# Kernel tuning notes

Hardware: AMD Instinct MI355X
Metric: run time of the kernel (lower is better)

## Reference

```python
import jax, jax.numpy as jnp
import numpy as np

N = 100000          # nodes
E = 3200000         # edges (avg degree 32)
F_IN = 128          # num_features
HID = 128           # hidden_channels
C = 8               # num_classes
G = 64              # graphs in batch
EPS = 1e-5


def setup_inputs() -> dict:
    key = jax.random.key(0)
    ks = jax.random.split(key, 10)
    x = jax.random.normal(ks[0], (N, F_IN), dtype=jnp.float32)
    edge_index = jax.random.randint(ks[1], (2, E), 0, N, dtype=jnp.int64)
    batch = jnp.sort(jax.random.randint(ks[2], (N,), 0, G, dtype=jnp.int64))
    # parameters
    glorot1 = float(np.sqrt(6.0 / (F_IN + HID)))
    W1 = jax.random.uniform(ks[3], (F_IN, HID), minval=-glorot1, maxval=glorot1, dtype=jnp.float32)
    conv1_bias = jnp.zeros((HID,), jnp.float32)
    bn_weight = jnp.ones((F_IN,), jnp.float32)
    bn_bias = jnp.zeros((F_IN,), jnp.float32)
    ln_weight = jnp.ones((HID,), jnp.float32)
    ln_bias = jnp.zeros((HID,), jnp.float32)
    glorot2 = float(np.sqrt(6.0 / (HID + C)))
    lin_W = jax.random.uniform(ks[4], (C, HID), minval=-glorot2, maxval=glorot2, dtype=jnp.float32)
    lin_b = jnp.zeros((C,), jnp.float32)
    return {"x": x, "edge_index": edge_index, "batch": batch,
            "bn_weight": bn_weight, "bn_bias": bn_bias,
            "W1": W1, "conv1_bias": conv1_bias,
            "ln_weight": ln_weight, "ln_bias": ln_bias,
            "lin_W": lin_W, "lin_b": lin_b}


def reference(x, edge_index, batch, bn_weight, bn_bias, W1, conv1_bias,
              ln_weight, ln_bias, lin_W, lin_b):
    n = x.shape[0]
    # BatchNorm1d over nodes (training-mode batch statistics, biased var)
    mu = x.mean(axis=0)
    var = x.var(axis=0)
    x = (x - mu) * jax.lax.rsqrt(var + EPS) * bn_weight + bn_bias
    # GCNConv: linear transform, add self-loops, symmetric normalization, scatter-add
    h = x @ W1                                   # [N, HID]
    loops = jnp.arange(n, dtype=edge_index.dtype)
    row = jnp.concatenate([edge_index[0], loops])  # source nodes
    col = jnp.concatenate([edge_index[1], loops])  # target nodes
    deg = jax.ops.segment_sum(jnp.ones_like(col, dtype=h.dtype), col, num_segments=N)
    dinv = jax.lax.rsqrt(deg)                    # deg >= 1 due to self-loops
    norm = dinv[row] * dinv[col]                 # [E+N]
    msg = h[row] * norm[:, None]                 # gather + scale
    h = jax.ops.segment_sum(msg, col, num_segments=N) + conv1_bias
    h = jax.nn.relu(h)
    # PyG LayerNorm, mode='graph', batch=None: normalize over the whole tensor
    h = h - h.mean()
    h = h * jax.lax.rsqrt(h.var() + EPS)
    h = h * ln_weight + ln_bias
    # global mean pool per graph
    counts = jax.ops.segment_sum(jnp.ones((n,), h.dtype), batch, num_segments=G)
    sums = jax.ops.segment_sum(h, batch, num_segments=G)
    g = sums / jnp.maximum(counts, 1.0)[:, None]  # [G, HID]
    return g @ lin_W.T + lin_b                    # [G, C]
```

## Files before the change

kernel.cpp:

```cpp
#include <hip/hip_runtime.h>

#define NN 100000
#define NE 3200000
#define F 128
#define NG 64
#define NC 8
#define EPSF 1e-5f

#define AGG_BLOCKS 25000
#define LDSTRIDE 136
#define BN_BLOCKS 1024

#define NBK 256
#define BNODES 391
#define BCAP 14336
#define CHUNK 4096
#define P1_BLOCKS ((NE + CHUNK - 1) / CHUNK)

typedef __attribute__((ext_vector_type(8))) short bf16x8;
typedef __attribute__((ext_vector_type(4))) float f32x4;
typedef _Float16 f16x2 __attribute__((ext_vector_type(2)));

union U32H2 { unsigned int u; f16x2 h; };
__device__ __forceinline__ f16x2 asH2(unsigned int u) { U32H2 c; c.u = u; return c.h; }
__device__ __forceinline__ unsigned int asU32(f16x2 h) { U32H2 c; c.h = h; return c.u; }

__device__ __forceinline__ unsigned short f2bf(float f) {
    unsigned int u = __float_as_uint(f);
    u = u + 0x7FFFu + ((u >> 16) & 1u);
    return (unsigned short)(u >> 16);
}
__device__ __forceinline__ unsigned short f2h_bits(float f) {
    union { _Float16 h; unsigned short u; } c;
    c.h = (_Float16)f;
    return c.u;
}

__global__ void bn_partial_k(const float* __restrict__ x, float* __restrict__ part,
                             int n, int rpb) {
    int tid = threadIdx.x, col = tid & 127, half = tid >> 7;
    int r0 = blockIdx.x * rpb, r1 = min(n, r0 + rpb);
    float s = 0.f, ss = 0.f;
    for (int r = r0 + half; r < r1; r += 2) {
        float v = x[(size_t)r * F + col];
        s += v; ss += v * v;
    }
    __shared__ float sh[512];
    sh[tid] = s; sh[256 + tid] = ss;
    __syncthreads();
    if (half == 0) {
        part[blockIdx.x * 256 + col]       = sh[col] + sh[col + 128];
        part[blockIdx.x * 256 + 128 + col] = sh[256 + col] + sh[256 + col + 128];
    }
}

__global__ void bn_finalize_k(const float* __restrict__ part,
                              const float* __restrict__ bnw, const float* __restrict__ bnb,
                              float* __restrict__ scale, float* __restrict__ shift, int n) {
    int col = blockIdx.x, tid = threadIdx.x;
    float s = 0.f, ss = 0.f;
    #pragma unroll
    for (int i = 0; i < 4; ++i) {
        int b = tid + i * 256;
        s  += part[b * 256 + col];
        ss += part[b * 256 + 128 + col];
    }
    __shared__ float shs[256], shss[256];
    shs[tid] = s; shss[tid] = ss;
    __syncthreads();
    for (int o = 128; o > 0; o >>= 1) {
        if (tid < o) { shs[tid] += shs[tid + o]; shss[tid] += shss[tid + o]; }
        __syncthreads();
    }
    if (tid == 0) {
        float mu  = shs[0] / (float)n;
        float var = shss[0] / (float)n - mu * mu;
        float rstd = rsqrtf(var + EPSF);
        float sc = bnw[col] * rstd;
        scale[col] = sc;
        shift[col] = bnb[col] - mu * sc;
    }
}

__global__ void prep_wpT_k(const float* __restrict__ W1, const float* __restrict__ scale,
                           unsigned short* __restrict__ WpT) {
    int idx = blockIdx.x * 256 + threadIdx.x;
    if (idx < F * F) {
        int k = idx >> 7, j = idx & 127;
        WpT[j * F + k] = f2bf(scale[k] * W1[idx]);
    }
}
__global__ void prep_s_k(const float* __restrict__ W1, const float* __restrict__ shift,
                         float* __restrict__ S) {
    int j = blockIdx.x, k = threadIdx.x;
    __shared__ float sh[128];
    sh[k] = shift[k] * W1[k * F + j];
    __syncthreads();
    for (int o = 64; o > 0; o >>= 1) {
        if (k < o) sh[k] += sh[k + o];
        __syncthreads();
    }
    if (k == 0) S[j] = sh[0];
}

__global__ __launch_bounds__(256) void bucket_k(const int* __restrict__ ei,
                                                int* __restrict__ bcur,
                                                unsigned int* __restrict__ bbuf) {
    __shared__ int cntl[NBK];
    __shared__ int basel[NBK];
    __shared__ int gbase[NBK];
    __shared__ unsigned int ent[CHUNK];
    __shared__ unsigned char bid[CHUNK];
    int tid = threadIdx.x;
    int e0 = blockIdx.x * CHUNK;
    int ecnt = min(NE - e0, CHUNK);
    cntl[tid] = 0;
    __syncthreads();
    int myr[16], myc[16], myl[16];
    #pragma unroll
    for (int k = 0; k < 16; ++k) {
        int i = tid + k * 256;
        if (i < ecnt) {
            int r = ei[e0 + i];
            int c = ei[NE + e0 + i];
            myr[k] = r; myc[k] = c;
            myl[k] = atomicAdd(&cntl[(unsigned)c / BNODES], 1);
        } else { myr[k] = -1; myc[k] = 0; myl[k] = 0; }
    }
    __syncthreads();
    int myv = cntl[tid];
    basel[tid] = myv;
    __syncthreads();
    for (int o = 1; o < 256; o <<= 1) {
        int t = (tid >= o) ? basel[tid - o] : 0;
        __syncthreads();
        basel[tid] += t;
        __syncthreads();
    }
    basel[tid] -= myv;
    gbase[tid] = atomicAdd(&bcur[tid], myv);
    __syncthreads();
    #pragma unroll
    for (int k = 0; k < 16; ++k) {
        if (myr[k] >= 0) {
            int b = (unsigned)myc[k] / BNODES;
            int s = basel[b] + myl[k];
            ent[s] = ((unsigned)myr[k] << 9) | (unsigned)(myc[k] - b * BNODES);
            bid[s] = (unsigned char)b;
        }
    }
    __syncthreads();
    for (int s = tid; s < ecnt; s += 256) {
        unsigned int v = ent[s];
        int b = bid[s];
        int idx = s - basel[b] + gbase[b];
        if (idx < BCAP) bbuf[(size_t)b * BCAP + idx] = v;
    }
}

__global__ void bbase_k(const int* __restrict__ bcur, int* __restrict__ bbase,
                        int* __restrict__ offs) {
    int tid = threadIdx.x;
    __shared__ int s[256];
    int v = bcur[tid];
    s[tid] = v;
    __syncthreads();
    for (int o = 1; o < 256; o <<= 1) {
        int t = (tid >= o) ? s[tid - o] : 0;
        __syncthreads();
        s[tid] += t;
        __syncthreads();
    }
    bbase[tid] = s[tid] - v;
    if (tid == 255) offs[NN] = s[255];
}

__global__ void hist2_k(const unsigned int* __restrict__ bbuf, const int* __restrict__ bcur,
                        const int* __restrict__ bbase,
                        int* __restrict__ offs, float* __restrict__ dinv) {
    int b = blockIdx.x, tid = threadIdx.x;
    __shared__ int h0[512], hA[512], hB[512];
    h0[tid] = 0; h0[tid + 256] = 0;
    __syncthreads();
    int m = min(bcur[b], BCAP);
    for (int i = tid; i < m; i += 256)
        atomicAdd(&h0[bbuf[(size_t)b * BCAP + i] & 511u], 1);
    __syncthreads();
    hA[tid] = h0[tid]; hA[tid + 256] = h0[tid + 256];
    __syncthreads();
    int* src = hA; int* dst = hB;
    for (int o = 1; o < 512; o <<= 1) {
        int i0 = tid, i1 = tid + 256;
        dst[i0] = src[i0] + ((i0 >= o) ? src[i0 - o] : 0);
        dst[i1] = src[i1] + ((i1 >= o) ? src[i1 - o] : 0);
        __syncthreads();
        int* tmp = src; src = dst; dst = tmp;
    }
    int nbase = b * BNODES;
    int base = bbase[b];
    int lim = min(BNODES, NN - nbase);
    for (int i = tid; i < lim; i += 256) {
        int d = h0[i];
        offs[nbase + i] = base + src[i] - d;
        dinv[nbase + i] = rsqrtf((float)d + 1.0f);
    }
}

__global__ void scatter2_k(const unsigned int* __restrict__ bbuf, const int* __restrict__ bcur,
                           const int* __restrict__ offs, int* __restrict__ srow) {
    int b = blockIdx.x, tid = threadIdx.x;
    __shared__ int cur[BNODES];
    for (int i = tid; i < BNODES; i += 256) cur[i] = 0;
    __syncthreads();
    int nbase = b * BNODES;
    int m = min(bcur[b], BCAP);
    for (int i = tid; i < m; i += 256) {
        unsigned int v = bbuf[(size_t)b * BCAP + i];
        int dstl = (int)(v & 511u);
        int pos = offs[nbase + dstl] + atomicAdd(&cur[dstl], 1);
        srow[pos] = (int)(v >> 9);
    }
}

__global__ __launch_bounds__(256) void gemm_k(const float* __restrict__ x,
                                              const unsigned short* __restrict__ WpT,
                                              const float* __restrict__ S,
                                              const float* __restrict__ dinv,
                                              unsigned short* __restrict__ hf, int n) {
    __shared__ unsigned short wt[128 * LDSTRIDE];
    __shared__ unsigned short xt[64 * LDSTRIDE];
    int tid = threadIdx.x;
    int row0 = blockIdx.x * 64;
    for (int i = tid; i < 2048; i += 256) {
        int r = i >> 4, c = (i & 15) * 8;
        uint4 v = *(const uint4*)&WpT[r * F + c];
        *(uint4*)&wt[r * LDSTRIDE + c] = v;
    }
    for (int i = tid; i < 2048; i += 256) {
        int r = i >> 5, c = (i & 31) * 4;
        float4 v = make_float4(0.f, 0.f, 0.f, 0.f);
        if (row0 + r < n) v = *(const float4*)&x[(size_t)(row0 + r) * F + c];
        unsigned int p0 = (unsigned int)f2bf(v.x) | ((unsigned int)f2bf(v.y) << 16);
        unsigned int p1 = (unsigned int)f2bf(v.z) | ((unsigned int)f2bf(v.w) << 16);
        *(uint2*)&xt[r * LDSTRIDE + c] = make_uint2(p0, p1);
    }
    __syncthreads();
    int wv = tid >> 6, lane = tid & 63;
    int lm = lane & 15, lk = lane >> 4;
    bf16x8 afrag[4];
    #pragma unroll
    for (int kk = 0; kk < 4; ++kk)
        afrag[kk] = *(bf16x8*)&xt[(wv * 16 + lm) * LDSTRIDE + kk * 32 + lk * 8];
    float dv[4];
    #pragma unroll
    for (int j = 0; j < 4; ++j) {
        int r = row0 + wv * 16 + lk * 4 + j;
        dv[j] = (r < n) ? dinv[r] : 1.0f;
    }
    #pragma unroll
    for (int nt = 0; nt < 8; ++nt) {
        float sv = S[nt * 16 + lm];
        f32x4 acc = {sv, sv, sv, sv};
        #pragma unroll
        for (int kk = 0; kk < 4; ++kk) {
            bf16x8 b = *(bf16x8*)&wt[(nt * 16 + lm) * LDSTRIDE + kk * 32 + lk * 8];
            acc = __builtin_amdgcn_mfma_f32_16x16x32_bf16(afrag[kk], b, acc, 0, 0, 0);
        }
        #pragma unroll
        for (int j = 0; j < 4; ++j) {
            int r = row0 + wv * 16 + lk * 4 + j;
            if (r < n) hf[(size_t)r * F + nt * 16 + lm] = f2h_bits(acc[j] * dv[j]);
        }
    }
}

__global__ __launch_bounds__(256) void agg_k(const uint4* __restrict__ hb4,
                                             const int* __restrict__ srow,
                                             const int* __restrict__ offs,
                                             const float* __restrict__ dinv,
                                             const float* __restrict__ bias,
                                             uint4* __restrict__ h2p4,
                                             float* __restrict__ lnpart, int n) {
    int lane = threadIdx.x & 63, wv = threadIdx.x >> 6;
    int node = blockIdx.x * 4 + wv;
    int cg = lane & 15;
    int sub = lane >> 4;
    float s_part = 0.f, ss_part = 0.f;
    if (node < n) {
        int st = offs[node], en = offs[node + 1];
        float di = dinv[node];
        f16x2 a0 = {0.f16, 0.f16}, a1 = a0, a2 = a0, a3 = a0;
        if (sub == 0) {
            uint4 qs = hb4[(size_t)node * 16 + cg];
            a0 += asH2(qs.x); a1 += asH2(qs.y); a2 += asH2(qs.z); a3 += asH2(qs.w);
        }
        const uint4 qz = make_uint4(0u, 0u, 0u, 0u);
        for (int base = st; base < en; base += 64) {
            int m = en - base; if (m > 64) m = 64;
            int sv = (lane < m) ? srow[base + lane] : 0;
            int nq = (m + 3) >> 2;
            int k = 0;
            for (; k + 2 <= nq; k += 2) {
                int i0 = 4 * k + sub, i1 = i0 + 4;
                int sr0 = __shfl(sv, i0), sr1 = __shfl(sv, i1);
                bool v0 = i0 < m, v1 = i1 < m;
                uint4 q0 = hb4[(size_t)(v0 ? sr0 : node) * 16 + cg];
                uint4 q1 = hb4[(size_t)(v1 ? sr1 : node) * 16 + cg];
                if (!v0) q0 = qz;
                if (!v1) q1 = qz;
                a0 += asH2(q0.x); a1 += asH2(q0.y); a2 += asH2(q0.z); a3 += asH2(q0.w);
                a0 += asH2(q1.x); a1 += asH2(q1.y); a2 += asH2(q1.z); a3 += asH2(q1.w);
            }
            for (; k < nq; ++k) {
                int i0 = 4 * k + sub;
                int sr0 = __shfl(sv, i0);
                bool v0 = i0 < m;
                uint4 q0 = hb4[(size_t)(v0 ? sr0 : node) * 16 + cg];
                if (!v0) q0 = qz;
                a0 += asH2(q0.x); a1 += asH2(q0.y); a2 += asH2(q0.z); a3 += asH2(q0.w);
            }
        }
        a0 += asH2((unsigned int)__shfl_xor((int)asU32(a0), 16));
        a1 += asH2((unsigned int)__shfl_xor((int)asU32(a1), 16));
        a2 += asH2((unsigned int)__shfl_xor((int)asU32(a2), 16));
        a3 += asH2((unsigned int)__shfl_xor((int)asU32(a3), 16));
        a0 += asH2((unsigned int)__shfl_xor((int)asU32(a0), 32));
        a1 += asH2((unsigned int)__shfl_xor((int)asU32(a1), 32));
        a2 += asH2((unsigned int)__shfl_xor((int)asU32(a2), 32));
        a3 += asH2((unsigned int)__shfl_xor((int)asU32(a3), 32));
        float acc[8] = {(float)a0[0], (float)a0[1], (float)a1[0], (float)a1[1],
                        (float)a2[0], (float)a2[1], (float)a3[0], (float)a3[1]};
        float4 b0 = *(const float4*)&bias[cg * 8];
        float4 b1 = *(const float4*)&bias[cg * 8 + 4];
        float bv[8] = {b0.x, b0.y, b0.z, b0.w, b1.x, b1.y, b1.z, b1.w};
        float r[8];
        #pragma unroll
        for (int j = 0; j < 8; ++j) r[j] = fmaxf(fmaf(acc[j], di, bv[j]), 0.f);
        if (sub == 0) {
            uint4 p;
            p.x = asU32(f16x2{(_Float16)r[0], (_Float16)r[1]});
            p.y = asU32(f16x2{(_Float16)r[2], (_Float16)r[3]});
            p.z = asU32(f16x2{(_Float16)r[4], (_Float16)r[5]});
            p.w = asU32(f16x2{(_Float16)r[6], (_Float16)r[7]});
            h2p4[(size_t)node * 16 + cg] = p;
            #pragma unroll
            for (int j = 0; j < 8; ++j) {
                s_part += r[j];
                ss_part += r[j] * r[j];
            }
        }
    }
    __shared__ float sh[512];
    sh[threadIdx.x] = s_part; sh[256 + threadIdx.x] = ss_part;
    __syncthreads();
    for (int o = 128; o > 0; o >>= 1) {
        if (threadIdx.x < o) {
            sh[threadIdx.x] += sh[threadIdx.x + o];
            sh[256 + threadIdx.x] += sh[256 + threadIdx.x + o];
        }
        __syncthreads();
    }
    if (threadIdx.x == 0) {
        lnpart[blockIdx.x * 2]     = sh[0];
        lnpart[blockIdx.x * 2 + 1] = sh[256];
    }
}

__global__ void ln_reduce_k(const float* __restrict__ lnpart, int nb,
                            float* __restrict__ lnstats) {
    int tid = threadIdx.x;
    double s = 0.0, ss = 0.0;
    for (int i = tid; i < nb; i += 256) {
        s  += (double)lnpart[2 * i];
        ss += (double)lnpart[2 * i + 1];
    }
    __shared__ double sh[512];
    sh[tid] = s; sh[256 + tid] = ss;
    __syncthreads();
    for (int o = 128; o > 0; o >>= 1) {
        if (tid < o) { sh[tid] += sh[tid + o]; sh[256 + tid] += sh[256 + tid + o]; }
        __syncthreads();
    }
    if (tid == 0) {
        double cnt = (double)NN * (double)F;
        double mu = sh[0] / cnt;
        double var = sh[256] / cnt - mu * mu;
        lnstats[0] = (float)mu;
        lnstats[1] = (float)(1.0 / sqrt(var + (double)EPSF));
    }
}

__global__ void pool1_k(const unsigned int* __restrict__ h2p, const int* __restrict__ batch,
                        float* __restrict__ gsum, int n) {
    int tid = threadIdx.x, cp = tid & 63, half = tid >> 6;
    int n0 = blockIdx.x * 256, n1 = min(n, n0 + 256);
    int r = n0 + half;
    if (r >= n1) return;
    int gcur = batch[r];
    float a0 = 0.f, a1 = 0.f;
    for (; r < n1; r += 4) {
        int g = batch[r];
        f16x2 hp = asH2(h2p[(size_t)r * 64 + cp]);
        if (g != gcur) {
            atomicAdd(&gsum[gcur * F + cp * 2], a0);
            atomicAdd(&gsum[gcur * F + cp * 2 + 1], a1);
            a0 = a1 = 0.f; gcur = g;
        }
        a0 += (float)hp[0];
        a1 += (float)hp[1];
    }
    atomicAdd(&gsum[gcur * F + cp * 2], a0);
    atomicAdd(&gsum[gcur * F + cp * 2 + 1], a1);
}

__global__ void pool2_k(const float* __restrict__ gsum, const int* __restrict__ batch,
                        const float* __restrict__ lnstats,
                        const float* __restrict__ lnw, const float* __restrict__ lnb,
                        const float* __restrict__ linW, const float* __restrict__ linb,
                        float* __restrict__ out, int n) {
    int g = blockIdx.x, tid = threadIdx.x;
    __shared__ int bounds[2];
    if (tid < 2) {
        int target = g + tid;
        int lo = 0, hi = n;
        while (lo < hi) {
            int mid = (lo + hi) >> 1;
            if (batch[mid] < target) lo = mid + 1; else hi = mid;
        }
        bounds[tid] = lo;
    }
    __syncthreads();
    int cg = bounds[1] - bounds[0];
    __shared__ float vals[128];
    float v = 0.f;
    if (cg > 0) {
        float m = gsum[g * F + tid] / (float)cg;
        v = (m - lnstats[0]) * lnstats[1] * lnw[tid] + lnb[tid];
    }
    vals[tid] = v;
    __syncthreads();
    if (tid < NC) {
        float o = linb[tid];
        for (int k = 0; k < F; ++k) o = fmaf(vals[k], linW[tid * F + k], o);
        out[g * NC + tid] = o;
    }
}

extern "C" void kernel_launch(void* const* d_in, const int* in_sizes, int n_in,
                              void* d_out, int out_size, void* d_ws, size_t ws_size,
                              hipStream_t stream) {
    const float* x     = (const float*)d_in[0];
    const int*   ei    = (const int*)d_in[1];
    const int*   batch = (const int*)d_in[2];
    const float* bnw   = (const float*)d_in[3];
    const float* bnb   = (const float*)d_in[4];
    const float* W1    = (const float*)d_in[5];
    const float* cbias = (const float*)d_in[6];
    const float* lnw   = (const float*)d_in[7];
    const float* lnb   = (const float*)d_in[8];
    const float* linW  = (const float*)d_in[9];
    const float* linb  = (const float*)d_in[10];
    float* out = (float*)d_out;

    char* w = (char*)d_ws;
    size_t used = 0;
    auto alloc = [&](size_t bytes) {
        char* p = w;
        size_t pad = (bytes + 255) & ~(size_t)255;
        w += pad;
        used += pad;
        return p;
    };
    size_t bucket_bytes = (size_t)NBK * BCAP * 4;
    size_t hf_bytes     = (size_t)NN * F * 2;
    char* regionA = (char*)alloc(bucket_bytes > hf_bytes ? bucket_bytes : hf_bytes);
    unsigned int*   bbuf = (unsigned int*)regionA;
    unsigned short* hf   = (unsigned short*)regionA;

    unsigned int* h2p = (unsigned int*)alloc((size_t)NN * F * 2);
    int*   srow    = (int*)alloc((size_t)NE * 4);
    int*   offs    = (int*)alloc((size_t)(NN + 1) * 4);
    float* dinv    = (float*)alloc((size_t)NN * 4);
    int*   bcur    = (int*)alloc(NBK * 4);
    int*   bbase   = (int*)alloc(NBK * 4);
    float* bnpart  = (float*)alloc((size_t)BN_BLOCKS * 256 * 4);
    float* scale   = (float*)alloc(512);
    float* shift   = (float*)alloc(512);
    unsigned short* WpT = (unsigned short*)alloc(128 * 128 * 2);
    float* Svec    = (float*)alloc(512);
    float* lnpart  = (float*)alloc((size_t)AGG_BLOCKS * 2 * 4);
    float* lnstats = (float*)alloc(256);
    float* gsum    = (float*)alloc((size_t)NG * F * 4);

    if (used > ws_size) {
        hipMemsetAsync(d_out, 0, (size_t)out_size * 4, stream);
        return;
    }

    hipMemsetAsync(bcur, 0, NBK * 4, stream);
    hipMemsetAsync(gsum, 0, (size_t)NG * F * 4, stream);

    int rpb = (NN + BN_BLOCKS - 1) / BN_BLOCKS;
    bn_partial_k<<<BN_BLOCKS, 256, 0, stream>>>(x, bnpart, NN, rpb);
    bn_finalize_k<<<128, 256, 0, stream>>>(bnpart, bnw, bnb, scale, shift, NN);
    prep_wpT_k<<<64, 256, 0, stream>>>(W1, scale, WpT);
    prep_s_k<<<128, 128, 0, stream>>>(W1, shift, Svec);

    bucket_k<<<P1_BLOCKS, 256, 0, stream>>>(ei, bcur, bbuf);
    bbase_k<<<1, 256, 0, stream>>>(bcur, bbase, offs);
    hist2_k<<<NBK, 256, 0, stream>>>(bbuf, bcur, bbase, offs, dinv);
    scatter2_k<<<NBK, 256, 0, stream>>>(bbuf, bcur, offs, srow);

    gemm_k<<<(NN + 63) / 64, 256, 0, stream>>>(x, WpT, Svec, dinv, hf, NN);
    agg_k<<<AGG_BLOCKS, 256, 0, stream>>>((const uint4*)hf, srow, offs, dinv,
                                          cbias, (uint4*)h2p, lnpart, NN);
    ln_reduce_k<<<1, 256, 0, stream>>>(lnpart, AGG_BLOCKS, lnstats);
    pool1_k<<<(NN + 255) / 256, 256, 0, stream>>>(h2p, batch, gsum, NN);
    pool2_k<<<NG, 128, 0, stream>>>(gsum, batch, lnstats, lnw, lnb, linW, linb, out, NN);
}
```

Measured before the change: 293.8 us.

## Split aggregation feature columns across XCD halves for better L2 locality

The aggregation kernel now splits each node's 128 feature columns into two 64-column halves, handled by different blocks. Blocks are mapped so that XCDs 0-3 handle the first half and 4-7 the second, which halves each XCD's working set of gathered rows in its private L2. Each wave processes 8 edges per step with 8 lanes per row instead of 16. The cost is twice as many blocks, duplicated index and offset reads, and more LayerNorm partials to reduce.

After: 321.1 us. 9.3% more time.

```diff
diff --git a/kernel.cpp b/kernel.cpp
--- a/kernel.cpp
+++ b/kernel.cpp
@@ -7,7 +7,7 @@
 #define NC 8
 #define EPSF 1e-5f
 
-#define AGG_BLOCKS 25000
+#define AGG2_BLOCKS 50000
 #define LDSTRIDE 136
 #define BN_BLOCKS 1024
 
@@ -282,56 +282,60 @@
                                              uint4* __restrict__ h2p4,
                                              float* __restrict__ lnpart, int n) {
     int lane = threadIdx.x & 63, wv = threadIdx.x >> 6;
-    int node = blockIdx.x * 4 + wv;
-    int cg = lane & 15;
-    int sub = lane >> 4;
+    int xcd = blockIdx.x & 7;
+    int half = xcd >> 2;
+    int idx = (blockIdx.x >> 3) * 4 + (xcd & 3);
+    int node = idx * 4 + wv;
+    int cg = lane & 7;
+    int sub = lane >> 3;
     float s_part = 0.f, ss_part = 0.f;
     if (node < n) {
         int st = offs[node], en = offs[node + 1];
         float di = dinv[node];
+        size_t rb = (size_t)half * 8 + cg;
         f16x2 a0 = {0.f16, 0.f16}, a1 = a0, a2 = a0, a3 = a0;
         if (sub == 0) {
-            uint4 qs = hb4[(size_t)node * 16 + cg];
+            uint4 qs = hb4[(size_t)node * 16 + rb];
             a0 += asH2(qs.x); a1 += asH2(qs.y); a2 += asH2(qs.z); a3 += asH2(qs.w);
         }
         const uint4 qz = make_uint4(0u, 0u, 0u, 0u);
         for (int base = st; base < en; base += 64) {
             int m = en - base; if (m > 64) m = 64;
             int sv = (lane < m) ? srow[base + lane] : 0;
-            int nq = (m + 3) >> 2;
+            int nq = (m + 7) >> 3;
             int k = 0;
             for (; k + 2 <= nq; k += 2) {
-                int i0 = 4 * k + sub, i1 = i0 + 4;
+                int i0 = 8 * k + sub, i1 = i0 + 8;
                 int sr0 = __shfl(sv, i0), sr1 = __shfl(sv, i1);
                 bool v0 = i0 < m, v1 = i1 < m;
-                uint4 q0 = hb4[(size_t)(v0 ? sr0 : node) * 16 + cg];
-                uint4 q1 = hb4[(size_t)(v1 ? sr1 : node) * 16 + cg];
+                uint4 q0 = hb4[(size_t)(v0 ? sr0 : node) * 16 + rb];
+                uint4 q1 = hb4[(size_t)(v1 ? sr1 : node) * 16 + rb];
                 if (!v0) q0 = qz;
                 if (!v1) q1 = qz;
                 a0 += asH2(q0.x); a1 += asH2(q0.y); a2 += asH2(q0.z); a3 += asH2(q0.w);
                 a0 += asH2(q1.x); a1 += asH2(q1.y); a2 += asH2(q1.z); a3 += asH2(q1.w);
             }
             for (; k < nq; ++k) {
-                int i0 = 4 * k + sub;
+                int i0 = 8 * k + sub;
                 int sr0 = __shfl(sv, i0);
                 bool v0 = i0 < m;
-                uint4 q0 = hb4[(size_t)(v0 ? sr0 : node) * 16 + cg];
+                uint4 q0 = hb4[(size_t)(v0 ? sr0 : node) * 16 + rb];
                 if (!v0) q0 = qz;
                 a0 += asH2(q0.x); a1 += asH2(q0.y); a2 += asH2(q0.z); a3 += asH2(q0.w);
             }
         }
-        a0 += asH2((unsigned int)__shfl_xor((int)asU32(a0), 16));
-        a1 += asH2((unsigned int)__shfl_xor((int)asU32(a1), 16));
-        a2 += asH2((unsigned int)__shfl_xor((int)asU32(a2), 16));
-        a3 += asH2((unsigned int)__shfl_xor((int)asU32(a3), 16));
-        a0 += asH2((unsigned int)__shfl_xor((int)asU32(a0), 32));
-        a1 += asH2((unsigned int)__shfl_xor((int)asU32(a1), 32));
-        a2 += asH2((unsigned int)__shfl_xor((int)asU32(a2), 32));
-        a3 += asH2((unsigned int)__shfl_xor((int)asU32(a3), 32));
+        #pragma unroll
+        for (int o = 8; o <= 32; o <<= 1) {
+            a0 += asH2((unsigned int)__shfl_xor((int)asU32(a0), o));
+            a1 += asH2((unsigned int)__shfl_xor((int)asU32(a1), o));
+            a2 += asH2((unsigned int)__shfl_xor((int)asU32(a2), o));
+            a3 += asH2((unsigned int)__shfl_xor((int)asU32(a3), o));
+        }
         float acc[8] = {(float)a0[0], (float)a0[1], (float)a1[0], (float)a1[1],
                         (float)a2[0], (float)a2[1], (float)a3[0], (float)a3[1]};
-        float4 b0 = *(const float4*)&bias[cg * 8];
-        float4 b1 = *(const float4*)&bias[cg * 8 + 4];
+        const float* bcol = &bias[half * 64 + cg * 8];
+        float4 b0 = *(const float4*)&bcol[0];
+        float4 b1 = *(const float4*)&bcol[4];
         float bv[8] = {b0.x, b0.y, b0.z, b0.w, b1.x, b1.y, b1.z, b1.w};
         float r[8];
         #pragma unroll
@@ -342,7 +346,7 @@
             p.y = asU32(f16x2{(_Float16)r[2], (_Float16)r[3]});
             p.z = asU32(f16x2{(_Float16)r[4], (_Float16)r[5]});
             p.w = asU32(f16x2{(_Float16)r[6], (_Float16)r[7]});
-            h2p4[(size_t)node * 16 + cg] = p;
+            h2p4[(size_t)node * 16 + rb] = p;
             #pragma unroll
             for (int j = 0; j < 8; ++j) {
                 s_part += r[j];
@@ -488,7 +492,7 @@
     float* shift   = (float*)alloc(512);
     unsigned short* WpT = (unsigned short*)alloc(128 * 128 * 2);
     float* Svec    = (float*)alloc(512);
-    float* lnpart  = (float*)alloc((size_t)AGG_BLOCKS * 2 * 4);
+    float* lnpart  = (float*)alloc((size_t)AGG2_BLOCKS * 2 * 4);
     float* lnstats = (float*)alloc(256);
     float* gsum    = (float*)alloc((size_t)NG * F * 4);
 
@@ -512,9 +516,9 @@
     scatter2_k<<<NBK, 256, 0, stream>>>(bbuf, bcur, offs, srow);
 
     gemm_k<<<(NN + 63) / 64, 256, 0, stream>>>(x, WpT, Svec, dinv, hf, NN);
-    agg_k<<<AGG_BLOCKS, 256, 0, stream>>>((const uint4*)hf, srow, offs, dinv,
-                                          cbias, (uint4*)h2p, lnpart, NN);
-    ln_reduce_k<<<1, 256, 0, stream>>>(lnpart, AGG_BLOCKS, lnstats);
+    agg_k<<<AGG2_BLOCKS, 256, 0, stream>>>((const uint4*)hf, srow, offs, dinv,
+                                           cbias, (uint4*)h2p, lnpart, NN);
+    ln_reduce_k<<<1, 256, 0, stream>>>(lnpart, AGG2_BLOCKS, lnstats);
     pool1_k<<<(NN + 255) / 256, 256, 0, stream>>>(h2p, batch, gsum, NN);
     pool2_k<<<NG, 128, 0, stream>>>(gsum, batch, lnstats, lnw, lnb, linW, linb, out, NN);
 }
```
